# Performance work log

Measured on AMD Instinct MI355X. Metric: run time of the kernel, lower is better.

## Reference

```python
import jax, jax.numpy as jnp
import numpy as np

IS_CAUSAL = True


def setup_inputs() -> dict:
    key = jax.random.key(0)
    kq, kk, kv = jax.random.split(key, 3)
    q = jax.random.normal(kq, (2, 32, 2048, 128), dtype=jnp.float32)
    k = jax.random.normal(kk, (2, 8, 2048, 128), dtype=jnp.float32)
    v = jax.random.normal(kv, (2, 8, 2048, 128), dtype=jnp.float32)
    return {"q": q, "k": k, "v": v}


def reference(q, k, v):
    # q: [B, Hq, Sq, D]; k, v: [B, Hk, Sk, D] with Hq % Hk == 0 (GQA)
    B, Hq, Sq, D = q.shape
    Hk, Sk = k.shape[1], k.shape[2]
    rep = Hq // Hk
    # GQA broadcast: repeat_interleave along head dim
    k_e = jnp.repeat(k, rep, axis=1)  # [B, Hq, Sk, D]
    v_e = jnp.repeat(v, rep, axis=1)
    scale = jnp.float32(1.0 / np.sqrt(D))
    # scores in fp32 (original casts s to float32 before softmax)
    s = jnp.einsum('bhqd,bhkd->bhqk', q, k_e).astype(jnp.float32) * scale
    if IS_CAUSAL:
        mask = jnp.tril(jnp.ones((Sq, Sk), dtype=bool))  # [Sq, Sk]
        s = jnp.where(mask, s, -jnp.inf)
    p = jax.nn.softmax(s, axis=-1).astype(q.dtype)  # [B, Hq, Sq, Sk]
    attn = jnp.einsum('bhqk,bhkd->bhqd', p, v_e)
    return attn
```

## Files before the change

### kernel.cpp

```cpp
#include <hip/hip_runtime.h>


typedef __bf16 bf16_t;
typedef __bf16 bf16x2 __attribute__((ext_vector_type(2)));
typedef __bf16 bf16x8 __attribute__((ext_vector_type(8)));
typedef float f32x4v __attribute__((ext_vector_type(4)));
typedef float f32x16 __attribute__((ext_vector_type(16)));
typedef unsigned int u32;
typedef u32 u32x4 __attribute__((ext_vector_type(4)));

constexpr int B_ = 2, HQ = 32, HK = 8, SQ = 2048, D = 128;
constexpr int QT = 128, KT = 32;
constexpr int NQT = SQ / QT;
constexpr int NT = SQ / KT;
constexpr int TILE_ELEM = KT * D * 2;
constexpr size_t TILE_BYTES = TILE_ELEM * 2;
constexpr size_t WS_NEED = (size_t)B_ * HK * NT * TILE_BYTES;

__device__ __forceinline__ u32 pkbf(float a, float b) {
  bf16x2 t; t[0] = (bf16_t)a; t[1] = (bf16_t)b;
  return __builtin_bit_cast(u32, t);
}
__device__ __forceinline__ float fexp2(float x) { return __builtin_exp2f(x); }

__device__ __forceinline__ void gl_lds16(const void* g, void* l) {
  __builtin_amdgcn_global_load_lds(
      (const __attribute__((address_space(1))) u32*)g,
      (__attribute__((address_space(3))) u32*)l, 16, 0, 0);
}

__global__ __launch_bounds__(256)
void prepass(const float* __restrict__ kg, const float* __restrict__ vg,
             bf16_t* __restrict__ ws) {
  const int blk = blockIdx.x;
  const int bh = blk >> 6, t = blk & 63;
  const float* ksrc = kg + ((size_t)bh * SQ + (size_t)t * KT) * D;
  const float* vsrc = vg + ((size_t)bh * SQ + (size_t)t * KT) * D;
  bf16_t* kdst = ws + (size_t)blk * TILE_ELEM;
  bf16_t* vdst = kdst + KT * D;
  const int tid = threadIdx.x;
#pragma unroll
  for (int i = 0; i < 2; ++i) {
    const int c = tid + 256 * i;
    const int r = c >> 4, p = c & 15, q = p ^ (r & 15);
    const float* s = ksrc + (size_t)r * D + 8 * q;
    f32x4v a = *(const f32x4v*)s;
    f32x4v b = *(const f32x4v*)(s + 4);
    bf16x8 w;
    w[0]=(bf16_t)a[0]; w[1]=(bf16_t)a[1]; w[2]=(bf16_t)a[2]; w[3]=(bf16_t)a[3];
    w[4]=(bf16_t)b[0]; w[5]=(bf16_t)b[1]; w[6]=(bf16_t)b[2]; w[7]=(bf16_t)b[3];
    *(bf16x8*)(kdst + (size_t)r * D + 8 * p) = w;
  }
#pragma unroll
  for (int i = 0; i < 2; ++i) {
    const int c = tid + 256 * i;
    const int d = c >> 2, p = c & 3, q = p ^ (d & 3);
    bf16x8 w;
#pragma unroll
    for (int j = 0; j < 8; ++j) w[j] = (bf16_t)vsrc[(size_t)(8 * q + j) * D + d];
    *(bf16x8*)(vdst + (size_t)d * KT + 8 * p) = w;
  }
}

__global__ __launch_bounds__(256, 4)
void fa4(const float* __restrict__ qg_, const bf16_t* __restrict__ ws,
         float* __restrict__ og_) {
  __shared__ __align__(16) char ldsraw[2 * TILE_BYTES];

  const int idx = blockIdx.x;
  const int g = idx >> 6, bh = idx & 63;
  const int qt = (NQT - 1) - g;
  const int b = bh >> 5, h = bh & 31, hk = h >> 2;

  const int tid = threadIdx.x;
  const int wv = tid >> 6, lane = tid & 63;
  const int ln = lane & 31, hx = lane >> 5;

  const int q0 = qt * QT;
  const float* qg = qg_ + ((size_t)(b * HQ + h) * SQ + q0) * D;
  float*       og = og_ + ((size_t)(b * HQ + h) * SQ + q0) * D;
  const bf16_t* wsrc = ws + (size_t)(b * HK + hk) * NT * TILE_ELEM;

  auto stage = [&](int t, int buf) {
    const char* src = (const char*)(wsrc + (size_t)t * TILE_ELEM);
    char* dst = ldsraw + (size_t)buf * TILE_BYTES;
#pragma unroll
    for (int i = 0; i < 4; ++i) {
      const int chunk = 4 * wv + i;
      gl_lds16(src + chunk * 1024 + lane * 16, dst + chunk * 1024);
    }
  };

  stage(0, 0);

  const float qscale = 0.08838834764831845f * 1.4426950408889634f;

  bf16x8 qf[8];
  {
    const float* qrp = qg + (size_t)(32 * wv + ln) * D + 8 * hx;
#pragma unroll
    for (int s = 0; s < 8; ++s) {
      f32x4v a = *(const f32x4v*)(qrp + 16 * s);
      f32x4v c = *(const f32x4v*)(qrp + 16 * s + 4);
      bf16x8 t;
      t[0]=(bf16_t)(a[0]*qscale); t[1]=(bf16_t)(a[1]*qscale);
      t[2]=(bf16_t)(a[2]*qscale); t[3]=(bf16_t)(a[3]*qscale);
      t[4]=(bf16_t)(c[0]*qscale); t[5]=(bf16_t)(c[1]*qscale);
      t[6]=(bf16_t)(c[2]*qscale); t[7]=(bf16_t)(c[3]*qscale);
      qf[s] = t;
    }
  }

  f32x16 Oa[4];
#pragma unroll
  for (int mb = 0; mb < 4; ++mb)
#pragma unroll
    for (int r = 0; r < 16; ++r) Oa[mb][r] = 0.f;
  float m = -1e30f, l = 0.f;

  const int wrow = q0 + 32 * wv;
  const int ntile = q0 / KT + 4;

  __syncthreads();

  int cur = 0;
  for (int ti = 0; ti < ntile; ++ti) {
    const int kb = ti * KT;
    if (ti + 1 < ntile) stage(ti + 1, cur ^ 1);

    if (kb <= wrow) {
      const bf16_t* kbp = (const bf16_t*)(ldsraw + (size_t)cur * TILE_BYTES);
      const bf16_t* vbp = kbp + KT * D;

      f32x16 sa;
#pragma unroll
      for (int r = 0; r < 16; ++r) sa[r] = 0.f;
      __builtin_amdgcn_s_setprio(1);
#pragma unroll
      for (int s = 0; s < 8; ++s) {
        const int cb = (2 * s + hx) ^ (ln & 15);
        bf16x8 kf = *(const bf16x8*)(kbp + ln * 128 + cb * 8);
        sa = __builtin_amdgcn_mfma_f32_32x32x16_bf16(kf, qf[s], sa, 0, 0, 0);
      }
      __builtin_amdgcn_s_setprio(0);

      if (kb == wrow) {
#pragma unroll
        for (int r = 0; r < 16; ++r) {
          const int kl = (r & 3) + 8 * (r >> 2) + 4 * hx;
          if (kl > ln) sa[r] = -1e30f;
        }
      }

      float tm = -1e30f;
#pragma unroll
      for (int r = 0; r < 16; ++r) tm = fmaxf(tm, sa[r]);
      tm = fmaxf(tm, __shfl_xor(tm, 32, 64));
      if (__any(tm > m + 8.f)) {
        const float mn = fmaxf(m, tm);
        const float corr = fexp2(m - mn);
        m = mn; l *= corr;
#pragma unroll
        for (int mb = 0; mb < 4; ++mb)
#pragma unroll
          for (int r = 0; r < 16; ++r) Oa[mb][r] *= corr;
      }
#pragma unroll
      for (int r = 0; r < 16; ++r) sa[r] = fexp2(sa[r] - m);
      float ps = 0.f;
#pragma unroll
      for (int r = 0; r < 16; ++r) ps += sa[r];
      ps += __shfl_xor(ps, 32, 64);
      l += ps;

      u32x4 pa[2];
#pragma unroll
      for (int s2 = 0; s2 < 2; ++s2) {
        const u32 A0 = pkbf(sa[8*s2+0], sa[8*s2+1]);
        const u32 A1 = pkbf(sa[8*s2+2], sa[8*s2+3]);
        const u32 B0 = pkbf(sa[8*s2+4], sa[8*s2+5]);
        const u32 B1 = pkbf(sa[8*s2+6], sa[8*s2+7]);
        const u32 sA0 = __shfl_xor(A0, 32, 64), sA1 = __shfl_xor(A1, 32, 64);
        const u32 sB0 = __shfl_xor(B0, 32, 64), sB1 = __shfl_xor(B1, 32, 64);
        pa[s2][0] = hx ? sB0 : A0;
        pa[s2][1] = hx ? sB1 : A1;
        pa[s2][2] = hx ? B0 : sA0;
        pa[s2][3] = hx ? B1 : sA1;
      }

      __builtin_amdgcn_s_setprio(1);
#pragma unroll
      for (int s2 = 0; s2 < 2; ++s2) {
#pragma unroll
        for (int mb = 0; mb < 4; ++mb) {
          const int d0 = ln + 32 * mb;
          const int cb = (2 * s2 + hx) ^ (d0 & 3);
          bf16x8 vf = *(const bf16x8*)(vbp + d0 * KT + cb * 8);
          Oa[mb] = __builtin_amdgcn_mfma_f32_32x32x16_bf16(
              vf, __builtin_bit_cast(bf16x8, pa[s2]), Oa[mb], 0, 0, 0);
        }
      }
      __builtin_amdgcn_s_setprio(0);
    }

    __syncthreads();
    cur ^= 1;
  }

  const float inv = 1.f / l;
  float* wlds = (float*)ldsraw + wv * 2048;
#pragma unroll
  for (int h2 = 0; h2 < 2; ++h2) {
#pragma unroll
    for (int mb2 = 0; mb2 < 2; ++mb2) {
      const int mb = 2 * h2 + mb2;
#pragma unroll
      for (int g2 = 0; g2 < 4; ++g2) {
        f32x4v v4;
        v4[0] = Oa[mb][4*g2+0] * inv; v4[1] = Oa[mb][4*g2+1] * inv;
        v4[2] = Oa[mb][4*g2+2] * inv; v4[3] = Oa[mb][4*g2+3] * inv;
        const int lslot = 2 * g2 + hx + 8 * mb2;
        const int pslot = lslot ^ (ln & 15);
        *(f32x4v*)(wlds + ln * 64 + pslot * 4) = v4;
      }
    }
    asm volatile("s_waitcnt lgkmcnt(0)" ::: "memory");
    __builtin_amdgcn_sched_barrier(0);
#pragma unroll
    for (int i = 0; i < 8; ++i) {
      const int q2 = 4 * i + (lane >> 4);
      const int lsl = lane & 15;
      const int psl = lsl ^ (q2 & 15);
      f32x4v v4 = *(const f32x4v*)(wlds + q2 * 64 + psl * 4);
      *(f32x4v*)(og + (size_t)(32 * wv + q2) * D + 64 * h2 + 4 * lsl) = v4;
    }
    __builtin_amdgcn_sched_barrier(0);
  }
}

namespace fb {
typedef float f32x4 __attribute__((ext_vector_type(4)));
constexpr int QT2 = 128, KT2 = 64;
constexpr int KELEM = 64 * 128, VELEM = 128 * 64, BUFE = KELEM + VELEM;

__device__ __forceinline__ u32 bfb(float f) {
  u32 u = __float_as_uint(f);
  u += 0x7fffu + ((u >> 16) & 1u);
  return u >> 16;
}
__device__ __forceinline__ bf16_t f2bf(float f) {
  unsigned short hs = (unsigned short)bfb(f);
  bf16_t b; __builtin_memcpy(&b, &hs, 2); return b;
}

__global__ __launch_bounds__(256, 2)
void fa2(const float* __restrict__ qg_, const float* __restrict__ kg_,
         const float* __restrict__ vg_, float* __restrict__ og_)
{
  __shared__ __align__(16) char ldsraw[2 * BUFE * 2];
  bf16_t* lds = (bf16_t*)ldsraw;
  const int qt = (int)gridDim.x - 1 - (int)blockIdx.x;
  const int bh = blockIdx.y;
  const int b = bh >> 5, h = bh & 31, hk = h >> 2;
  const int tid = threadIdx.x;
  const int wv = tid >> 6, lane = tid & 63;
  const int ln = lane & 31, hx = lane >> 5;
  const int q0 = qt * QT2;
  const float* qg = qg_ + ((size_t)(b * HQ + h) * SQ + q0) * D;
  const float* kg = kg_ + (size_t)(b * HK + hk) * SQ * D;
  const float* vg = vg_ + (size_t)(b * HK + hk) * SQ * D;
  float*       og = og_ + ((size_t)(b * HQ + h) * SQ + q0) * D;
  const float qscale = 0.08838834764831845f * 1.4426950408889634f;
  bf16x8 qf[8];
  {
    const float* qrow = qg + (size_t)(32 * wv + ln) * D;
#pragma unroll
    for (int s = 0; s < 8; ++s) {
      const float* p = qrow + 16 * s + 8 * hx;
      f32x4 a = *(const f32x4*)p;
      f32x4 c = *(const f32x4*)(p + 4);
      bf16x8 t;
      t[0]=f2bf(a[0]*qscale); t[1]=f2bf(a[1]*qscale);
      t[2]=f2bf(a[2]*qscale); t[3]=f2bf(a[3]*qscale);
      t[4]=f2bf(c[0]*qscale); t[5]=f2bf(c[1]*qscale);
      t[6]=f2bf(c[2]*qscale); t[7]=f2bf(c[3]*qscale);
      qf[s] = t;
    }
  }
  f32x16 Oa[4];
#pragma unroll
  for (int mb = 0; mb < 4; ++mb)
#pragma unroll
    for (int r = 0; r < 16; ++r) Oa[mb][r] = 0.f;
  float m = -1e30f, l = 0.f;
  const int qrow_g = q0 + 32 * wv + ln;
  const int wlast = q0 + 32 * wv + 31;
  const int kv_end = q0 + QT2;
  const int krow = tid >> 2, kq = tid & 3;
  const int vkh = tid & 7, vd4 = tid >> 3;
  f32x4 kst[8], vst[8];
  auto kstage_load = [&](int kb) {
    const float* src = kg + (size_t)(kb + krow) * D + kq * 32;
#pragma unroll
    for (int it = 0; it < 4; ++it) {
      kst[2*it]   = *(const f32x4*)(src + 8 * it);
      kst[2*it+1] = *(const f32x4*)(src + 8 * it + 4);
    }
  };
  auto kstage_write = [&](int buf) {
    bf16_t* kbp = lds + buf * BUFE;
#pragma unroll
    for (int it = 0; it < 4; ++it) {
      const int cb = (kq * 4 + it) ^ (krow & 7);
      bf16x8 w;
      w[0]=f2bf(kst[2*it][0]);   w[1]=f2bf(kst[2*it][1]);
      w[2]=f2bf(kst[2*it][2]);   w[3]=f2bf(kst[2*it][3]);
      w[4]=f2bf(kst[2*it+1][0]); w[5]=f2bf(kst[2*it+1][1]);
      w[6]=f2bf(kst[2*it+1][2]); w[7]=f2bf(kst[2*it+1][3]);
      *(bf16x8*)(kbp + krow * 128 + cb * 8) = w;
    }
  };
  auto vstage_load = [&](int kb) {
    const float* src = vg + (size_t)(kb + 8 * vkh) * D + 4 * vd4;
#pragma unroll
    for (int i = 0; i < 8; ++i) vst[i] = *(const f32x4*)(src + (size_t)i * D);
  };
  auto vstage_write = [&](int buf) {
    bf16_t* vbp = lds + buf * BUFE + KELEM;
#pragma unroll
    for (int j = 0; j < 4; ++j) {
      const int d = 4 * vd4 + j;
      const int cb = vkh ^ (d & 7);
      bf16x8 w;
#pragma unroll
      for (int i = 0; i < 8; ++i) w[i] = f2bf(vst[i][j]);
      *(bf16x8*)(vbp + d * 64 + cb * 8) = w;
    }
  };
  kstage_load(0); kstage_write(0);
  vstage_load(0); vstage_write(0);
  __syncthreads();
  int cur = 0;
  for (int kb = 0; kb < kv_end; kb += KT2) {
    const bool nx = (kb + KT2 < kv_end);
    const bool act = (kb <= wlast);
    if (nx) kstage_load(kb + KT2);
    u32x4 pa[4];
    if (act) {
      const bf16_t* kbp = lds + cur * BUFE;
      f32x16 s0, s1;
#pragma unroll
      for (int r = 0; r < 16; ++r) { s0[r] = 0.f; s1[r] = 0.f; }
#pragma unroll
      for (int s = 0; s < 8; ++s) {
        const int cb = (2 * s + hx) ^ (ln & 7);
        bf16x8 k0 = *(const bf16x8*)(kbp + ln * 128 + cb * 8);
        bf16x8 k1 = *(const bf16x8*)(kbp + (ln + 32) * 128 + cb * 8);
        s0 = __builtin_amdgcn_mfma_f32_32x32x16_bf16(k0, qf[s], s0, 0, 0, 0);
        s1 = __builtin_amdgcn_mfma_f32_32x32x16_bf16(k1, qf[s], s1, 0, 0, 0);
      }
      if (kb + 63 > q0 + 32 * wv) {
#pragma unroll
        for (int r = 0; r < 16; ++r) {
          const int kl = (r & 3) + 8 * (r >> 2) + 4 * hx;
          if (kb + kl > qrow_g)      s0[r] = -1e30f;
          if (kb + 32 + kl > qrow_g) s1[r] = -1e30f;
        }
      }
      float tm = -1e30f;
#pragma unroll
      for (int r = 0; r < 16; ++r) tm = fmaxf(tm, fmaxf(s0[r], s1[r]));
      tm = fmaxf(tm, __shfl_xor(tm, 32, 64));
      if (__any(tm > m + 8.f)) {
        const float mn = fmaxf(m, tm);
        const float corr = fexp2(m - mn);
        m = mn; l *= corr;
#pragma unroll
        for (int mb = 0; mb < 4; ++mb)
#pragma unroll
          for (int r = 0; r < 16; ++r) Oa[mb][r] *= corr;
      }
      f32x16 p0, p1;
#pragma unroll
      for (int r = 0; r < 16; ++r) {
        p0[r] = fexp2(s0[r] - m);
        p1[r] = fexp2(s1[r] - m);
      }
      float ps = 0.f;
#pragma unroll
      for (int r = 0; r < 16; ++r) ps += p0[r] + p1[r];
      ps += __shfl_xor(ps, 32, 64);
      l += ps;
#pragma unroll
      for (int kb2 = 0; kb2 < 2; ++kb2) {
        const f32x16& pp = kb2 ? p1 : p0;
#pragma unroll
        for (int s2 = 0; s2 < 2; ++s2) {
          const u32 A0 = pkbf(pp[8*s2+0], pp[8*s2+1]);
          const u32 A1 = pkbf(pp[8*s2+2], pp[8*s2+3]);
          const u32 B0 = pkbf(pp[8*s2+4], pp[8*s2+5]);
          const u32 B1 = pkbf(pp[8*s2+6], pp[8*s2+7]);
          const u32 sA0 = __shfl_xor(A0, 32, 64), sA1 = __shfl_xor(A1, 32, 64);
          const u32 sB0 = __shfl_xor(B0, 32, 64), sB1 = __shfl_xor(B1, 32, 64);
          const int ks = 2 * kb2 + s2;
          pa[ks][0] = hx ? sB0 : A0;
          pa[ks][1] = hx ? sB1 : A1;
          pa[ks][2] = hx ? B0 : sA0;
          pa[ks][3] = hx ? B1 : sA1;
        }
      }
    }
    if (nx) kstage_write(cur ^ 1);
    if (nx) vstage_load(kb + KT2);
    if (act) {
      const bf16_t* vbp = lds + cur * BUFE + KELEM;
#pragma unroll
      for (int mb = 0; mb < 4; ++mb) {
        const int d0 = ln + 32 * mb;
#pragma unroll
        for (int ks = 0; ks < 4; ++ks) {
          const int cb = (hx + 2 * ks) ^ (d0 & 7);
          bf16x8 vf = *(const bf16x8*)(vbp + d0 * 64 + cb * 8);
          Oa[mb] = __builtin_amdgcn_mfma_f32_32x32x16_bf16(
              vf, __builtin_bit_cast(bf16x8, pa[ks]), Oa[mb], 0, 0, 0);
        }
      }
    }
    if (nx) vstage_write(cur ^ 1);
    __syncthreads();
    cur ^= 1;
  }
  float* ol = (float*)ldsraw;
  float* wbase = ol + wv * 4096;
  const float inv = 1.f / l;
#pragma unroll
  for (int mb = 0; mb < 4; ++mb) {
#pragma unroll
    for (int g = 0; g < 4; ++g) {
      f32x4 v4;
      v4[0] = Oa[mb][4*g+0]*inv; v4[1] = Oa[mb][4*g+1]*inv;
      v4[2] = Oa[mb][4*g+2]*inv; v4[3] = Oa[mb][4*g+3]*inv;
      const int chunk = (2 * g + hx + 8 * mb) ^ (ln & 7);
      *(f32x4*)(wbase + ln * 128 + chunk * 4) = v4;
    }
  }
  __syncthreads();
#pragma unroll
  for (int i = 0; i < 16; ++i) {
    const int q2 = 2 * i + hx;
    const int cs = ln ^ (q2 & 7);
    f32x4 v4 = *(const f32x4*)(wbase + q2 * 128 + cs * 4);
    *(f32x4*)(og + (size_t)(32 * wv + q2) * D + 4 * ln) = v4;
  }
}
}

extern "C" void kernel_launch(void* const* d_in, const int* in_sizes, int n_in,
                              void* d_out, int out_size, void* d_ws, size_t ws_size,
                              hipStream_t stream) {
  const float* q = (const float*)d_in[0];
  const float* k = (const float*)d_in[1];
  const float* v = (const float*)d_in[2];
  float* out = (float*)d_out;
  if (ws_size >= WS_NEED) {
    prepass<<<dim3(B_ * HK * NT), 256, 0, stream>>>(k, v, (bf16_t*)d_ws);
    fa4<<<dim3(NQT * 64), 256, 0, stream>>>(q, (const bf16_t*)d_ws, out);
  } else {
    fb::fa2<<<dim3(SQ / fb::QT2, B_ * HQ), 256, 0, stream>>>(q, k, v, out);
  }
}
```

Measured before the change: 166.2 us.

## Split KV range across wave pairs with LDS merge of partial softmax

Query tile shrinks to 64 rows, and the four waves become two row-waves times two KV groups. Each KV group walks its own half of the causal key tiles, and the two partial (m, l, O) states are merged through LDS at the end. The aim is to shorten the per-block serial KV loop and raise block count and occupancy (launch bounds raised to 5 blocks per CU). In exchange it drops double-buffered prefetch, so each tile is loaded and then synchronised before compute, and it adds a merge epilogue. The P shuffle is also trimmed to two cross-lane exchanges per step.

Result: slower. 491.0 us (+195.4%).

```diff
diff --git a/kernel.cpp b/kernel.cpp
--- a/kernel.cpp
+++ b/kernel.cpp
@@ -10,7 +10,7 @@
 typedef u32 u32x4 __attribute__((ext_vector_type(4)));
 
 constexpr int B_ = 2, HQ = 32, HK = 8, SQ = 2048, D = 128;
-constexpr int QT = 128, KT = 32;
+constexpr int QT = 64, KT = 32;
 constexpr int NQT = SQ / QT;
 constexpr int NT = SQ / KT;
 constexpr int TILE_ELEM = KT * D * 2;
@@ -62,8 +62,8 @@
   }
 }
 
-__global__ __launch_bounds__(256, 4)
-void fa4(const float* __restrict__ qg_, const bf16_t* __restrict__ ws,
+__global__ __launch_bounds__(256, 5)
+void fa5(const float* __restrict__ qg_, const bf16_t* __restrict__ ws,
          float* __restrict__ og_) {
   __shared__ __align__(16) char ldsraw[2 * TILE_BYTES];
 
@@ -73,31 +73,34 @@
   const int b = bh >> 5, h = bh & 31, hk = h >> 2;
 
   const int tid = threadIdx.x;
-  const int wv = tid >> 6, lane = tid & 63;
+  const int wave = tid >> 6, lane = tid & 63;
   const int ln = lane & 31, hx = lane >> 5;
+  const int rw = wave & 1;
+  const int kg = wave >> 1;
 
   const int q0 = qt * QT;
   const float* qg = qg_ + ((size_t)(b * HQ + h) * SQ + q0) * D;
   float*       og = og_ + ((size_t)(b * HQ + h) * SQ + q0) * D;
   const bf16_t* wsrc = ws + (size_t)(b * HK + hk) * NT * TILE_ELEM;
 
-  auto stage = [&](int t, int buf) {
-    const char* src = (const char*)(wsrc + (size_t)t * TILE_ELEM);
-    char* dst = ldsraw + (size_t)buf * TILE_BYTES;
-#pragma unroll
-    for (int i = 0; i < 4; ++i) {
-      const int chunk = 4 * wv + i;
+  const int ntg = qt + 1;
+  const int tbase = kg * ntg;
+
+  auto stage = [&](int tl) {
+    const char* src = (const char*)(wsrc + (size_t)(tbase + tl) * TILE_ELEM);
+    char* dst = ldsraw + (size_t)kg * TILE_BYTES;
+#pragma unroll
+    for (int i = 0; i < 8; ++i) {
+      const int chunk = rw * 8 + i;
       gl_lds16(src + chunk * 1024 + lane * 16, dst + chunk * 1024);
     }
   };
-
-  stage(0, 0);
 
   const float qscale = 0.08838834764831845f * 1.4426950408889634f;
 
   bf16x8 qf[8];
   {
-    const float* qrp = qg + (size_t)(32 * wv + ln) * D + 8 * hx;
+    const float* qrp = qg + (size_t)(32 * rw + ln) * D + 8 * hx;
 #pragma unroll
     for (int s = 0; s < 8; ++s) {
       f32x4v a = *(const f32x4v*)(qrp + 16 * s);
@@ -118,18 +121,15 @@
     for (int r = 0; r < 16; ++r) Oa[mb][r] = 0.f;
   float m = -1e30f, l = 0.f;
 
-  const int wrow = q0 + 32 * wv;
-  const int ntile = q0 / KT + 4;
-
-  __syncthreads();
-
-  int cur = 0;
-  for (int ti = 0; ti < ntile; ++ti) {
-    const int kb = ti * KT;
-    if (ti + 1 < ntile) stage(ti + 1, cur ^ 1);
-
+  const int wrow = q0 + 32 * rw;
+
+  for (int ti = 0; ti < ntg; ++ti) {
+    stage(ti);
+    __syncthreads();
+
+    const int kb = (tbase + ti) * KT;
     if (kb <= wrow) {
-      const bf16_t* kbp = (const bf16_t*)(ldsraw + (size_t)cur * TILE_BYTES);
+      const bf16_t* kbp = (const bf16_t*)(ldsraw + (size_t)kg * TILE_BYTES);
       const bf16_t* vbp = kbp + KT * D;
 
       f32x16 sa;
@@ -180,12 +180,12 @@
         const u32 A1 = pkbf(sa[8*s2+2], sa[8*s2+3]);
         const u32 B0 = pkbf(sa[8*s2+4], sa[8*s2+5]);
         const u32 B1 = pkbf(sa[8*s2+6], sa[8*s2+7]);
-        const u32 sA0 = __shfl_xor(A0, 32, 64), sA1 = __shfl_xor(A1, 32, 64);
-        const u32 sB0 = __shfl_xor(B0, 32, 64), sB1 = __shfl_xor(B1, 32, 64);
-        pa[s2][0] = hx ? sB0 : A0;
-        pa[s2][1] = hx ? sB1 : A1;
-        pa[s2][2] = hx ? B0 : sA0;
-        pa[s2][3] = hx ? B1 : sA1;
+        const u32 r0 = __shfl_xor(hx ? A0 : B0, 32, 64);
+        const u32 r1 = __shfl_xor(hx ? A1 : B1, 32, 64);
+        pa[s2][0] = hx ? r0 : A0;
+        pa[s2][1] = hx ? r1 : A1;
+        pa[s2][2] = hx ? B0 : r0;
+        pa[s2][3] = hx ? B1 : r1;
       }
 
       __builtin_amdgcn_s_setprio(1);
@@ -204,37 +204,79 @@
     }
 
     __syncthreads();
-    cur ^= 1;
-  }
-
-  const float inv = 1.f / l;
-  float* wlds = (float*)ldsraw + wv * 2048;
-#pragma unroll
-  for (int h2 = 0; h2 < 2; ++h2) {
-#pragma unroll
-    for (int mb2 = 0; mb2 < 2; ++mb2) {
-      const int mb = 2 * h2 + mb2;
+  }
+
+  float* mlb = (float*)ldsraw;
+  if (kg) {
+    mlb[(rw * 64 + lane) * 2]     = m;
+    mlb[(rw * 64 + lane) * 2 + 1] = l;
+  }
+  __syncthreads();
+  float mB = -1e30f, lB = 0.f;
+  if (!kg) {
+    mB = mlb[(rw * 64 + lane) * 2];
+    lB = mlb[(rw * 64 + lane) * 2 + 1];
+  }
+  __syncthreads();
+  float* ob = (float*)ldsraw;
+  if (kg) {
+#pragma unroll
+    for (int mb = 0; mb < 4; ++mb)
 #pragma unroll
       for (int g2 = 0; g2 < 4; ++g2) {
         f32x4v v4;
-        v4[0] = Oa[mb][4*g2+0] * inv; v4[1] = Oa[mb][4*g2+1] * inv;
-        v4[2] = Oa[mb][4*g2+2] * inv; v4[3] = Oa[mb][4*g2+3] * inv;
-        const int lslot = 2 * g2 + hx + 8 * mb2;
-        const int pslot = lslot ^ (ln & 15);
-        *(f32x4v*)(wlds + ln * 64 + pslot * 4) = v4;
-      }
-    }
-    asm volatile("s_waitcnt lgkmcnt(0)" ::: "memory");
-    __builtin_amdgcn_sched_barrier(0);
-#pragma unroll
-    for (int i = 0; i < 8; ++i) {
-      const int q2 = 4 * i + (lane >> 4);
-      const int lsl = lane & 15;
-      const int psl = lsl ^ (q2 & 15);
-      f32x4v v4 = *(const f32x4v*)(wlds + q2 * 64 + psl * 4);
-      *(f32x4v*)(og + (size_t)(32 * wv + q2) * D + 64 * h2 + 4 * lsl) = v4;
-    }
-    __builtin_amdgcn_sched_barrier(0);
+        v4[0] = Oa[mb][4*g2+0]; v4[1] = Oa[mb][4*g2+1];
+        v4[2] = Oa[mb][4*g2+2]; v4[3] = Oa[mb][4*g2+3];
+        *(f32x4v*)(ob + rw * 4096 + (mb * 4 + g2) * 256 + lane * 4) = v4;
+      }
+  }
+  __syncthreads();
+  if (!kg) {
+    const float M  = fmaxf(m, mB);
+    const float cA = fexp2(m - M), cB = fexp2(mB - M);
+    l = l * cA + lB * cB;
+#pragma unroll
+    for (int mb = 0; mb < 4; ++mb)
+#pragma unroll
+      for (int g2 = 0; g2 < 4; ++g2) {
+        f32x4v v4 = *(const f32x4v*)(ob + rw * 4096 + (mb * 4 + g2) * 256 + lane * 4);
+#pragma unroll
+        for (int k = 0; k < 4; ++k)
+          Oa[mb][4*g2+k] = Oa[mb][4*g2+k] * cA + v4[k] * cB;
+      }
+  }
+  __syncthreads();
+
+  if (!kg) {
+    const float inv = 1.f / l;
+    float* wlds = (float*)ldsraw + rw * 2048;
+#pragma unroll
+    for (int h2 = 0; h2 < 2; ++h2) {
+#pragma unroll
+      for (int mb2 = 0; mb2 < 2; ++mb2) {
+        const int mb = 2 * h2 + mb2;
+#pragma unroll
+        for (int g2 = 0; g2 < 4; ++g2) {
+          f32x4v v4;
+          v4[0] = Oa[mb][4*g2+0] * inv; v4[1] = Oa[mb][4*g2+1] * inv;
+          v4[2] = Oa[mb][4*g2+2] * inv; v4[3] = Oa[mb][4*g2+3] * inv;
+          const int lslot = 2 * g2 + hx + 8 * mb2;
+          const int pslot = lslot ^ (ln & 15);
+          *(f32x4v*)(wlds + ln * 64 + pslot * 4) = v4;
+        }
+      }
+      asm volatile("s_waitcnt lgkmcnt(0)" ::: "memory");
+      __builtin_amdgcn_sched_barrier(0);
+#pragma unroll
+      for (int i = 0; i < 8; ++i) {
+        const int q2 = 4 * i + (lane >> 4);
+        const int lsl = lane & 15;
+        const int psl = lsl ^ (q2 & 15);
+        f32x4v v4 = *(const f32x4v*)(wlds + q2 * 64 + psl * 4);
+        *(f32x4v*)(og + (size_t)(32 * rw + q2) * D + 64 * h2 + 4 * lsl) = v4;
+      }
+      __builtin_amdgcn_sched_barrier(0);
+    }
   }
 }
 
@@ -464,7 +506,7 @@
   float* out = (float*)d_out;
   if (ws_size >= WS_NEED) {
     prepass<<<dim3(B_ * HK * NT), 256, 0, stream>>>(k, v, (bf16_t*)d_ws);
-    fa4<<<dim3(NQT * 64), 256, 0, stream>>>(q, (const bf16_t*)d_ws, out);
+    fa5<<<dim3(NQT * 64), 256, 0, stream>>>(q, (const bf16_t*)d_ws, out);
   } else {
     fb::fa2<<<dim3(SQ / fb::QT2, B_ * HQ), 256, 0, stream>>>(q, k, v, out);
   }
```

## Make attention kernel persistent with atomic work queue and triple-buffered K/V staging

Applied to the files above, without the earlier changes.

Replaces the one-block-per-tile grid with a persistent kernel of fixed block count that pulls (q-tile, head) work items from a global atomic counter, largest causal tiles first, to balance the triangular workload. K/V tiles are now triple-buffered with explicit vmcnt waits so loads run two tiles ahead, and one cross-lane shuffle pair per step is removed. It costs an extra memset launch, an atomic plus barrier per item, more LDS per block and a lower occupancy hint.

New measurement: 147.8 us. 11.1% less time.

```diff
diff --git a/kernel.cpp b/kernel.cpp
--- a/kernel.cpp
+++ b/kernel.cpp
@@ -13,9 +13,12 @@
 constexpr int QT = 128, KT = 32;
 constexpr int NQT = SQ / QT;
 constexpr int NT = SQ / KT;
+constexpr int NITEM = NQT * 64;
+constexpr int NBLK = 768;
 constexpr int TILE_ELEM = KT * D * 2;
 constexpr size_t TILE_BYTES = TILE_ELEM * 2;
-constexpr size_t WS_NEED = (size_t)B_ * HK * NT * TILE_BYTES;
+constexpr size_t WS_IMG = (size_t)B_ * HK * NT * TILE_BYTES;
+constexpr size_t WS_NEED = WS_IMG + 64;
 
 __device__ __forceinline__ u32 pkbf(float a, float b) {
   bf16x2 t; t[0] = (bf16_t)a; t[1] = (bf16_t)b;
@@ -62,179 +65,194 @@
   }
 }
 
-__global__ __launch_bounds__(256, 4)
-void fa4(const float* __restrict__ qg_, const bf16_t* __restrict__ ws,
-         float* __restrict__ og_) {
-  __shared__ __align__(16) char ldsraw[2 * TILE_BYTES];
-
-  const int idx = blockIdx.x;
-  const int g = idx >> 6, bh = idx & 63;
-  const int qt = (NQT - 1) - g;
-  const int b = bh >> 5, h = bh & 31, hk = h >> 2;
+__global__ __launch_bounds__(256, 3)
+void fa6(const float* __restrict__ qg_, const bf16_t* __restrict__ ws,
+         float* __restrict__ og_, int* __restrict__ cnt) {
+  __shared__ __align__(16) char ldsraw[3 * TILE_BYTES];
+  __shared__ int item_s;
 
   const int tid = threadIdx.x;
   const int wv = tid >> 6, lane = tid & 63;
   const int ln = lane & 31, hx = lane >> 5;
-
-  const int q0 = qt * QT;
-  const float* qg = qg_ + ((size_t)(b * HQ + h) * SQ + q0) * D;
-  float*       og = og_ + ((size_t)(b * HQ + h) * SQ + q0) * D;
-  const bf16_t* wsrc = ws + (size_t)(b * HK + hk) * NT * TILE_ELEM;
-
-  auto stage = [&](int t, int buf) {
-    const char* src = (const char*)(wsrc + (size_t)t * TILE_ELEM);
-    char* dst = ldsraw + (size_t)buf * TILE_BYTES;
-#pragma unroll
-    for (int i = 0; i < 4; ++i) {
-      const int chunk = 4 * wv + i;
-      gl_lds16(src + chunk * 1024 + lane * 16, dst + chunk * 1024);
-    }
-  };
-
-  stage(0, 0);
-
   const float qscale = 0.08838834764831845f * 1.4426950408889634f;
 
-  bf16x8 qf[8];
-  {
-    const float* qrp = qg + (size_t)(32 * wv + ln) * D + 8 * hx;
-#pragma unroll
-    for (int s = 0; s < 8; ++s) {
-      f32x4v a = *(const f32x4v*)(qrp + 16 * s);
-      f32x4v c = *(const f32x4v*)(qrp + 16 * s + 4);
-      bf16x8 t;
-      t[0]=(bf16_t)(a[0]*qscale); t[1]=(bf16_t)(a[1]*qscale);
-      t[2]=(bf16_t)(a[2]*qscale); t[3]=(bf16_t)(a[3]*qscale);
-      t[4]=(bf16_t)(c[0]*qscale); t[5]=(bf16_t)(c[1]*qscale);
-      t[6]=(bf16_t)(c[2]*qscale); t[7]=(bf16_t)(c[3]*qscale);
-      qf[s] = t;
-    }
-  }
-
-  f32x16 Oa[4];
-#pragma unroll
-  for (int mb = 0; mb < 4; ++mb)
-#pragma unroll
-    for (int r = 0; r < 16; ++r) Oa[mb][r] = 0.f;
-  float m = -1e30f, l = 0.f;
-
-  const int wrow = q0 + 32 * wv;
-  const int ntile = q0 / KT + 4;
-
-  __syncthreads();
-
-  int cur = 0;
-  for (int ti = 0; ti < ntile; ++ti) {
-    const int kb = ti * KT;
-    if (ti + 1 < ntile) stage(ti + 1, cur ^ 1);
-
-    if (kb <= wrow) {
-      const bf16_t* kbp = (const bf16_t*)(ldsraw + (size_t)cur * TILE_BYTES);
-      const bf16_t* vbp = kbp + KT * D;
-
-      f32x16 sa;
-#pragma unroll
-      for (int r = 0; r < 16; ++r) sa[r] = 0.f;
-      __builtin_amdgcn_s_setprio(1);
+  for (;;) {
+    if (tid == 0) item_s = atomicAdd(cnt, 1);
+    __syncthreads();
+    const int it = item_s;
+    if (it >= NITEM) break;
+
+    const int qt = (NQT - 1) - (it >> 6);
+    const int bh = it & 63;
+    const int b = bh >> 5, h = bh & 31, hk = h >> 2;
+    const int q0 = qt * QT;
+    const float* qg = qg_ + ((size_t)(b * HQ + h) * SQ + q0) * D;
+    float*       og = og_ + ((size_t)(b * HQ + h) * SQ + q0) * D;
+    const bf16_t* wsrc = ws + (size_t)(b * HK + hk) * NT * TILE_ELEM;
+    const int ntile = q0 / KT + 4;
+    const int wrow = q0 + 32 * wv;
+
+    auto stage = [&](int tl, int buf) {
+      const char* src = (const char*)(wsrc + (size_t)tl * TILE_ELEM);
+      char* dst = ldsraw + (size_t)buf * TILE_BYTES;
+#pragma unroll
+      for (int i = 0; i < 4; ++i) {
+        const int chunk = 4 * wv + i;
+        gl_lds16(src + chunk * 1024 + lane * 16, dst + chunk * 1024);
+      }
+    };
+
+    stage(0, 0);
+
+    bf16x8 qf[8];
+    {
+      const float* qrp = qg + (size_t)(32 * wv + ln) * D + 8 * hx;
 #pragma unroll
       for (int s = 0; s < 8; ++s) {
-        const int cb = (2 * s + hx) ^ (ln & 15);
-        bf16x8 kf = *(const bf16x8*)(kbp + ln * 128 + cb * 8);
-        sa = __builtin_amdgcn_mfma_f32_32x32x16_bf16(kf, qf[s], sa, 0, 0, 0);
-      }
-      __builtin_amdgcn_s_setprio(0);
-
-      if (kb == wrow) {
-#pragma unroll
-        for (int r = 0; r < 16; ++r) {
-          const int kl = (r & 3) + 8 * (r >> 2) + 4 * hx;
-          if (kl > ln) sa[r] = -1e30f;
-        }
-      }
-
-      float tm = -1e30f;
-#pragma unroll
-      for (int r = 0; r < 16; ++r) tm = fmaxf(tm, sa[r]);
-      tm = fmaxf(tm, __shfl_xor(tm, 32, 64));
-      if (__any(tm > m + 8.f)) {
-        const float mn = fmaxf(m, tm);
-        const float corr = fexp2(m - mn);
-        m = mn; l *= corr;
-#pragma unroll
-        for (int mb = 0; mb < 4; ++mb)
-#pragma unroll
-          for (int r = 0; r < 16; ++r) Oa[mb][r] *= corr;
-      }
-#pragma unroll
-      for (int r = 0; r < 16; ++r) sa[r] = fexp2(sa[r] - m);
-      float ps = 0.f;
-#pragma unroll
-      for (int r = 0; r < 16; ++r) ps += sa[r];
-      ps += __shfl_xor(ps, 32, 64);
-      l += ps;
-
-      u32x4 pa[2];
-#pragma unroll
-      for (int s2 = 0; s2 < 2; ++s2) {
-        const u32 A0 = pkbf(sa[8*s2+0], sa[8*s2+1]);
-        const u32 A1 = pkbf(sa[8*s2+2], sa[8*s2+3]);
-        const u32 B0 = pkbf(sa[8*s2+4], sa[8*s2+5]);
-        const u32 B1 = pkbf(sa[8*s2+6], sa[8*s2+7]);
-        const u32 sA0 = __shfl_xor(A0, 32, 64), sA1 = __shfl_xor(A1, 32, 64);
-        const u32 sB0 = __shfl_xor(B0, 32, 64), sB1 = __shfl_xor(B1, 32, 64);
-        pa[s2][0] = hx ? sB0 : A0;
-        pa[s2][1] = hx ? sB1 : A1;
-        pa[s2][2] = hx ? B0 : sA0;
-        pa[s2][3] = hx ? B1 : sA1;
-      }
-
-      __builtin_amdgcn_s_setprio(1);
-#pragma unroll
-      for (int s2 = 0; s2 < 2; ++s2) {
-#pragma unroll
-        for (int mb = 0; mb < 4; ++mb) {
-          const int d0 = ln + 32 * mb;
-          const int cb = (2 * s2 + hx) ^ (d0 & 3);
-          bf16x8 vf = *(const bf16x8*)(vbp + d0 * KT + cb * 8);
-          Oa[mb] = __builtin_amdgcn_mfma_f32_32x32x16_bf16(
-              vf, __builtin_bit_cast(bf16x8, pa[s2]), Oa[mb], 0, 0, 0);
-        }
-      }
-      __builtin_amdgcn_s_setprio(0);
-    }
-
-    __syncthreads();
-    cur ^= 1;
-  }
-
-  const float inv = 1.f / l;
-  float* wlds = (float*)ldsraw + wv * 2048;
-#pragma unroll
-  for (int h2 = 0; h2 < 2; ++h2) {
-#pragma unroll
-    for (int mb2 = 0; mb2 < 2; ++mb2) {
-      const int mb = 2 * h2 + mb2;
-#pragma unroll
-      for (int g2 = 0; g2 < 4; ++g2) {
-        f32x4v v4;
-        v4[0] = Oa[mb][4*g2+0] * inv; v4[1] = Oa[mb][4*g2+1] * inv;
-        v4[2] = Oa[mb][4*g2+2] * inv; v4[3] = Oa[mb][4*g2+3] * inv;
-        const int lslot = 2 * g2 + hx + 8 * mb2;
-        const int pslot = lslot ^ (ln & 15);
-        *(f32x4v*)(wlds + ln * 64 + pslot * 4) = v4;
-      }
-    }
+        f32x4v a = *(const f32x4v*)(qrp + 16 * s);
+        f32x4v c = *(const f32x4v*)(qrp + 16 * s + 4);
+        bf16x8 t;
+        t[0]=(bf16_t)(a[0]*qscale); t[1]=(bf16_t)(a[1]*qscale);
+        t[2]=(bf16_t)(a[2]*qscale); t[3]=(bf16_t)(a[3]*qscale);
+        t[4]=(bf16_t)(c[0]*qscale); t[5]=(bf16_t)(c[1]*qscale);
+        t[6]=(bf16_t)(c[2]*qscale); t[7]=(bf16_t)(c[3]*qscale);
+        qf[s] = t;
+      }
+    }
+    stage(1, 1);
+
+    f32x16 Oa[4];
+#pragma unroll
+    for (int mb = 0; mb < 4; ++mb)
+#pragma unroll
+      for (int r = 0; r < 16; ++r) Oa[mb][r] = 0.f;
+    float m = -1e30f, l = 0.f;
+
+    int cur = 0;
+    for (int t = 0; t < ntile; ++t) {
+      if (t + 1 < ntile) { asm volatile("s_waitcnt vmcnt(4)" ::: "memory"); }
+      else               { asm volatile("s_waitcnt vmcnt(0)" ::: "memory"); }
+      __builtin_amdgcn_sched_barrier(0);
+      __builtin_amdgcn_s_barrier();
+      __builtin_amdgcn_sched_barrier(0);
+
+      if (t + 2 < ntile) {
+        const int sb = (cur == 0) ? 2 : cur - 1;
+        stage(t + 2, sb);
+      }
+
+      const int kb = t * KT;
+      if (kb <= wrow) {
+        const bf16_t* kbp = (const bf16_t*)(ldsraw + (size_t)cur * TILE_BYTES);
+        const bf16_t* vbp = kbp + KT * D;
+
+        f32x16 sa;
+#pragma unroll
+        for (int r = 0; r < 16; ++r) sa[r] = 0.f;
+        __builtin_amdgcn_s_setprio(1);
+#pragma unroll
+        for (int s = 0; s < 8; ++s) {
+          const int cb = (2 * s + hx) ^ (ln & 15);
+          bf16x8 kf = *(const bf16x8*)(kbp + ln * 128 + cb * 8);
+          sa = __builtin_amdgcn_mfma_f32_32x32x16_bf16(kf, qf[s], sa, 0, 0, 0);
+        }
+        __builtin_amdgcn_s_setprio(0);
+
+        if (kb == wrow) {
+#pragma unroll
+          for (int r = 0; r < 16; ++r) {
+            const int kl = (r & 3) + 8 * (r >> 2) + 4 * hx;
+            if (kl > ln) sa[r] = -1e30f;
+          }
+        }
+
+        float tm = -1e30f;
+#pragma unroll
+        for (int r = 0; r < 16; ++r) tm = fmaxf(tm, sa[r]);
+        tm = fmaxf(tm, __shfl_xor(tm, 32, 64));
+        if (__any(tm > m + 8.f)) {
+          const float mn = fmaxf(m, tm);
+          const float corr = fexp2(m - mn);
+          m = mn; l *= corr;
+#pragma unroll
+          for (int mb = 0; mb < 4; ++mb)
+#pragma unroll
+            for (int r = 0; r < 16; ++r) Oa[mb][r] *= corr;
+        }
+#pragma unroll
+        for (int r = 0; r < 16; ++r) sa[r] = fexp2(sa[r] - m);
+        float ps = 0.f;
+#pragma unroll
+        for (int r = 0; r < 16; ++r) ps += sa[r];
+        ps += __shfl_xor(ps, 32, 64);
+        l += ps;
+
+        u32x4 pa[2];
+#pragma unroll
+        for (int s2 = 0; s2 < 2; ++s2) {
+          const u32 A0 = pkbf(sa[8*s2+0], sa[8*s2+1]);
+          const u32 A1 = pkbf(sa[8*s2+2], sa[8*s2+3]);
+          const u32 B0 = pkbf(sa[8*s2+4], sa[8*s2+5]);
+          const u32 B1 = pkbf(sa[8*s2+6], sa[8*s2+7]);
+          const u32 r0 = __shfl_xor(hx ? A0 : B0, 32, 64);
+          const u32 r1 = __shfl_xor(hx ? A1 : B1, 32, 64);
+          pa[s2][0] = hx ? r0 : A0;
+          pa[s2][1] = hx ? r1 : A1;
+          pa[s2][2] = hx ? B0 : r0;
+          pa[s2][3] = hx ? B1 : r1;
+        }
+
+        __builtin_amdgcn_s_setprio(1);
+#pragma unroll
+        for (int s2 = 0; s2 < 2; ++s2) {
+#pragma unroll
+          for (int mb = 0; mb < 4; ++mb) {
+            const int d0 = ln + 32 * mb;
+            const int cb = (2 * s2 + hx) ^ (d0 & 3);
+            bf16x8 vf = *(const bf16x8*)(vbp + d0 * KT + cb * 8);
+            Oa[mb] = __builtin_amdgcn_mfma_f32_32x32x16_bf16(
+                vf, __builtin_bit_cast(bf16x8, pa[s2]), Oa[mb], 0, 0, 0);
+          }
+        }
+        __builtin_amdgcn_s_setprio(0);
+      }
+
+      cur = (cur == 2) ? 0 : cur + 1;
+    }
+
     asm volatile("s_waitcnt lgkmcnt(0)" ::: "memory");
+    __builtin_amdgcn_s_barrier();
     __builtin_amdgcn_sched_barrier(0);
-#pragma unroll
-    for (int i = 0; i < 8; ++i) {
-      const int q2 = 4 * i + (lane >> 4);
-      const int lsl = lane & 15;
-      const int psl = lsl ^ (q2 & 15);
-      f32x4v v4 = *(const f32x4v*)(wlds + q2 * 64 + psl * 4);
-      *(f32x4v*)(og + (size_t)(32 * wv + q2) * D + 64 * h2 + 4 * lsl) = v4;
-    }
-    __builtin_amdgcn_sched_barrier(0);
+
+    const float inv = 1.f / l;
+    float* wlds = (float*)ldsraw + wv * 2048;
+#pragma unroll
+    for (int h2 = 0; h2 < 2; ++h2) {
+#pragma unroll
+      for (int mb2 = 0; mb2 < 2; ++mb2) {
+        const int mb = 2 * h2 + mb2;
+#pragma unroll
+        for (int g2 = 0; g2 < 4; ++g2) {
+          f32x4v v4;
+          v4[0] = Oa[mb][4*g2+0] * inv; v4[1] = Oa[mb][4*g2+1] * inv;
+          v4[2] = Oa[mb][4*g2+2] * inv; v4[3] = Oa[mb][4*g2+3] * inv;
+          const int lslot = 2 * g2 + hx + 8 * mb2;
+          const int pslot = lslot ^ (ln & 15);
+          *(f32x4v*)(wlds + ln * 64 + pslot * 4) = v4;
+        }
+      }
+      asm volatile("s_waitcnt lgkmcnt(0)" ::: "memory");
+      __builtin_amdgcn_sched_barrier(0);
+#pragma unroll
+      for (int i = 0; i < 8; ++i) {
+        const int q2 = 4 * i + (lane >> 4);
+        const int lsl = lane & 15;
+        const int psl = lsl ^ (q2 & 15);
+        f32x4v v4 = *(const f32x4v*)(wlds + q2 * 64 + psl * 4);
+        *(f32x4v*)(og + (size_t)(32 * wv + q2) * D + 64 * h2 + 4 * lsl) = v4;
+      }
+      __builtin_amdgcn_sched_barrier(0);
+    }
   }
 }
 
@@ -463,8 +481,10 @@
   const float* v = (const float*)d_in[2];
   float* out = (float*)d_out;
   if (ws_size >= WS_NEED) {
+    int* cnt = (int*)((char*)d_ws + WS_IMG);
+    hipMemsetAsync(cnt, 0, sizeof(int), stream);
     prepass<<<dim3(B_ * HK * NT), 256, 0, stream>>>(k, v, (bf16_t*)d_ws);
-    fa4<<<dim3(NQT * 64), 256, 0, stream>>>(q, (const bf16_t*)d_ws, out);
+    fa6<<<dim3(NBLK), 256, 0, stream>>>(q, (const bf16_t*)d_ws, out, cnt);
   } else {
     fb::fa2<<<dim3(SQ / fb::QT2, B_ * HQ), 256, 0, stream>>>(q, k, v, out);
   }
```
